# Optimization experiments

Hardware: AMD Instinct MI355X
Metric: run time of the kernel (lower is better)

Reference implementation:

```python
import jax, jax.numpy as jnp
import numpy as np
from jax import lax

NUM_HEADS = 8
EPS = 1e-5  # BatchNorm eps, eval mode with running_mean=0, running_var=1


def _dwconv3x3(x, w):
    # depthwise 3x3, stride 1, pad 1; x: [N,C,H,W], w: [C,1,3,3]
    return lax.conv_general_dilated(x, w, (1, 1), ((1, 1), (1, 1)),
                                    feature_group_count=x.shape[1],
                                    dimension_numbers=('NCHW', 'OIHW', 'NCHW'))


def _bn_eval(x, g, b):
    # eval BN with running stats (0,1): x * g/sqrt(1+eps) + b, channel dim 1
    s = (g * (1.0 / (1.0 + EPS) ** 0.5))
    return x * s[None, :, None, None] + b[None, :, None, None]


def setup_inputs() -> dict:
    key = jax.random.key(0)
    ks = jax.random.split(key, 10)
    B, h, w, C = 2, 16, 16, 128
    T = 1 + h * w
    H = NUM_HEADS
    inp = {
        'x': jax.random.normal(ks[0], (B, T, C), dtype=jnp.float32),
        'attn_score_grad': jax.random.normal(ks[1], (B, H, T, T), dtype=jnp.float32),
        # depthwise conv weights for q/k/v projections
        'dwq_w': jax.random.normal(ks[2], (C, 1, 3, 3), dtype=jnp.float32) * 0.1,
        'dwk_w': jax.random.normal(ks[3], (C, 1, 3, 3), dtype=jnp.float32) * 0.1,
        'dwv_w': jax.random.normal(ks[4], (C, 1, 3, 3), dtype=jnp.float32) * 0.1,
        'bnq_g': jnp.ones((C,), jnp.float32), 'bnq_b': jnp.zeros((C,), jnp.float32),
        'bnk_g': jnp.ones((C,), jnp.float32), 'bnk_b': jnp.zeros((C,), jnp.float32),
        'bnv_g': jnp.ones((C,), jnp.float32), 'bnv_b': jnp.zeros((C,), jnp.float32),
        # linear projections (qkv_bias=False)
        'Wq': jax.random.normal(ks[5], (C, C), dtype=jnp.float32) * (C ** -0.5),
        'Wk': jax.random.normal(ks[6], (C, C), dtype=jnp.float32) * (C ** -0.5),
        'Wv': jax.random.normal(ks[7], (C, C), dtype=jnp.float32) * (C ** -0.5),
        # conv_layer: Conv2d(2C->2C, k3, s2, p1) + BN
        'conv_w': jax.random.normal(ks[8], (2 * C, 2 * C, 3, 3), dtype=jnp.float32) * 0.02,
        'conv_b': jax.random.normal(ks[9], (2 * C,), dtype=jnp.float32) * 0.02,
        'bn2_g': jnp.ones((2 * C,), jnp.float32), 'bn2_b': jnp.zeros((2 * C,), jnp.float32),
        'h': 16, 'w': 16,
    }
    return inp


def reference(x, attn_score_grad, dwq_w, dwk_w, dwv_w, bnq_g, bnq_b, bnk_g, bnk_b,
              bnv_g, bnv_b, Wq, Wk, Wv, conv_w, conv_b, bn2_g, bn2_b, h, w):
    B, T, C = x.shape
    H = NUM_HEADS
    d = C // H
    scale = C ** -0.5  # note: full dim, as in the original

    # forward_conv: split cls token, depthwise conv + BN per q/k/v
    cls = x[:, :1]                                          # [B,1,C]
    xs = x[:, 1:].reshape(B, h, w, C).transpose(0, 3, 1, 2)  # [B,C,h,w]

    def conv_proj(dw, g, b):
        t = _bn_eval(_dwconv3x3(xs, dw), g, b)              # [B,C,h,w]
        return t.transpose(0, 2, 3, 1).reshape(B, h * w, C)

    q = jnp.concatenate([cls, conv_proj(dwq_w, bnq_g, bnq_b)], axis=1)
    k = jnp.concatenate([cls, conv_proj(dwk_w, bnk_g, bnk_b)], axis=1)
    v = jnp.concatenate([cls, conv_proj(dwv_w, bnv_g, bnv_b)], axis=1)

    # linear projections then split heads: b t (h d) -> b h t d
    q = (q @ Wq.T).reshape(B, T, H, d).transpose(0, 2, 1, 3)
    k = (k @ Wk.T).reshape(B, T, H, d).transpose(0, 2, 1, 3)
    v = (v @ Wv.T).reshape(B, T, H, d).transpose(0, 2, 1, 3)

    kv = jnp.concatenate([k, v], axis=-1)                   # [B,H,T,2d]

    # normalize attn_score_grad (temperature-softmax mixture on non-cls part)
    first = attn_score_grad[..., 0:1]
    rem = attn_score_grad[..., 1:]
    pos = jax.nn.softmax(rem / 0.5, axis=-1)
    neg = jax.nn.softmax(-rem / 0.5, axis=-1)
    score = jnp.concatenate([first, 0.7 * pos + 0.3 * (1.0 - neg)], axis=-1)  # [B,H,T,T]

    # weighted_kv[b,h,t1,t2,:] = score[b,h,t1,t2] * kv[b,h,t1,:]
    weighted = score[..., None] * kv[:, :, :, None, :]      # [B,H,T,T,2d]

    cls_tok = weighted[..., :1, :]                          # [B,H,T,1,2d]
    # raw row-major reshape (mixes head into channels), faithful to torch .reshape
    feat = weighted[..., 1:, :].reshape(B, T, h, w, 2 * C)  # [B,T,h,w,2C]
    ci = feat.transpose(0, 1, 4, 2, 3).reshape(B * T, 2 * C, h, w)

    co = lax.conv_general_dilated(ci, conv_w, (2, 2), ((1, 1), (1, 1)),
                                  dimension_numbers=('NCHW', 'OIHW', 'NCHW'))
    co = co + conv_b[None, :, None, None]
    co = _bn_eval(co, bn2_g, bn2_b)                         # [B*T,2C,h/2,w/2]

    co = co.reshape(B, T, H, 2 * d, h // 2, w // 2).transpose(0, 2, 1, 3, 4, 5)
    cf = co.reshape(B, H, T, (h // 2) * (w // 2), 2 * d)    # raw reshape, faithful

    kvps = jnp.concatenate([cls_tok, cf], axis=-2)          # [B,H,T,K,2d]
    k_ps = kvps[..., :d]                                    # [B,H,T,K,d]
    v_ps = kvps[..., d:]

    attn = jax.nn.softmax(jnp.einsum('bhtd,bhtkd->bhtk', q, k_ps) * scale, axis=-1)
    out = jnp.einsum('bhtk,bhtkd->bhtd', attn, v_ps)        # [B,H,T,d]
    out = out.transpose(0, 2, 1, 3).reshape(B, T, C)        # b h t d -> b t (h d)
    return jax.nn.gelu(out, approximate=False)
```

## Files before the change

### kernel.cpp

```cpp
#include <hip/hip_runtime.h>

#define BB 2
#define TT 257
#define CC 128
#define HH 8
#define DD 16
#define C2O 256
#define NIMG (BB*TT)
#define ROWS (BB*HH*TT)
#define KTOT 2304

static __device__ __forceinline__ float wred_max(float v) {
    #pragma unroll
    for (int off = 32; off; off >>= 1) v = fmaxf(v, __shfl_xor(v, off, 64));
    return v;
}
static __device__ __forceinline__ float wred_sum(float v) {
    #pragma unroll
    for (int off = 32; off; off >>= 1) v += __shfl_xor(v, off, 64);
    return v;
}

#define BN_INV 0.9999950000374997f

__global__ void k_pre(const float* __restrict__ x,
                      const float* __restrict__ dwq, const float* __restrict__ dwk, const float* __restrict__ dwv,
                      const float* __restrict__ gq, const float* __restrict__ bq,
                      const float* __restrict__ gk, const float* __restrict__ bk,
                      const float* __restrict__ gv, const float* __restrict__ bv,
                      float* __restrict__ pre) {
    int blk = blockIdx.x;
    int which = blk / NIMG;
    int it = blk - which * NIMG;
    int b = it / TT, t = it - b * TT;
    int c = threadIdx.x;
    const float* dw = (which == 0) ? dwq : (which == 1) ? dwk : dwv;
    const float* g  = (which == 0) ? gq  : (which == 1) ? gk  : gv;
    const float* bi = (which == 0) ? bq  : (which == 1) ? bk  : bv;
    float val;
    if (t == 0) {
        val = x[(b * TT) * CC + c];
    } else {
        int y = (t - 1) >> 4, xx = (t - 1) & 15;
        float s = 0.f;
        #pragma unroll
        for (int ky = 0; ky < 3; ky++) {
            int yy = y + ky - 1;
            if (yy < 0 || yy > 15) continue;
            #pragma unroll
            for (int kx = 0; kx < 3; kx++) {
                int xb = xx + kx - 1;
                if (xb < 0 || xb > 15) continue;
                s += dw[c * 9 + ky * 3 + kx] * x[(b * TT + 1 + yy * 16 + xb) * CC + c];
            }
        }
        val = s * (g[c] * BN_INV) + bi[c];
    }
    pre[(which * NIMG + it) * CC + c] = val;
}

__global__ void k_proj(const float* __restrict__ pre,
                       const float* __restrict__ Wq, const float* __restrict__ Wk, const float* __restrict__ Wv,
                       float* __restrict__ qh, float* __restrict__ kv) {
    int blk = blockIdx.x;
    int which = blk / NIMG;
    int it = blk - which * NIMG;
    int b = it / TT, t = it - b * TT;
    int o = threadIdx.x;
    __shared__ float row[CC];
    row[o] = pre[(which * NIMG + it) * CC + o];
    __syncthreads();
    const float* W = (which == 0) ? Wq : (which == 1) ? Wk : Wv;
    const float* wr = W + o * CC;
    float acc = 0.f;
    #pragma unroll 8
    for (int c = 0; c < CC; c++) acc += wr[c] * row[c];
    int hh = o >> 4, dd = o & 15;
    long ridx = (long)(b * HH + hh) * TT + t;
    if (which == 0)      qh[ridx * DD + dd] = acc;
    else if (which == 1) kv[ridx * 32 + dd] = acc;
    else                 kv[ridx * 32 + 16 + dd] = acc;
}

__global__ void k_score(const float* __restrict__ asg, float* __restrict__ score) {
    int wid = threadIdx.x >> 6;
    int lane = threadIdx.x & 63;
    int r = blockIdx.x * 4 + wid;
    if (r >= ROWS) return;
    const float* src = asg + (long)r * TT;
    float* dst = score + (long)r * TT;
    float e[4];
    #pragma unroll
    for (int i = 0; i < 4; i++) e[i] = src[1 + lane + 64 * i] * 2.0f;
    float mx = fmaxf(fmaxf(e[0], e[1]), fmaxf(e[2], e[3]));
    mx = wred_max(mx);
    float mn = fminf(fminf(e[0], e[1]), fminf(e[2], e[3]));
    mn = -wred_max(-mn);
    float pe[4], ne[4], ps = 0.f, ns = 0.f;
    #pragma unroll
    for (int i = 0; i < 4; i++) {
        pe[i] = expf(e[i] - mx); ps += pe[i];
        ne[i] = expf(mn - e[i]); ns += ne[i];
    }
    ps = wred_sum(ps); ns = wred_sum(ns);
    float rp = 1.f / ps, rn = 1.f / ns;
    #pragma unroll
    for (int i = 0; i < 4; i++)
        dst[1 + lane + 64 * i] = 0.7f * pe[i] * rp + 0.3f * (1.f - ne[i] * rn);
    if (lane == 0) dst[0] = src[0];
}

__global__ void k_w2(const float* __restrict__ cw, float* __restrict__ wt2) {
    int o = blockIdx.x;
    int t = threadIdx.x;
    for (int i = t; i < KTOT; i += 256) {
        int jp = i / 288;
        int r = i - jp * 288;
        int d = r >> 5, v = r & 31;
        wt2[o * KTOT + i] = cw[o * KTOT + (jp * 32 + v) * 9 + d];
    }
}

__launch_bounds__(256, 2)
__global__ void k_fconv(const float* __restrict__ wt2, const float* __restrict__ score,
                        const float* __restrict__ kv, const float* __restrict__ cb,
                        const float* __restrict__ g2, const float* __restrict__ b2,
                        float* __restrict__ cf) {
    __shared__ float s_S[8][256];
    __shared__ float s_kv[8][32];
    __shared__ float s_P[9][8][16][8];
    int bid = blockIdx.x;
    int oc  = bid / NIMG;
    int img = bid - oc * NIMG;
    int b = img / TT, tp = img - b * TT;
    int tid = threadIdx.x;

    {
        int j = tid >> 5, c = tid & 31;
        int m = tp * 8 + j;
        int hh = m / TT, t = m - hh * TT;
        long row = (long)(b * HH + hh) * TT + t;
        s_kv[j][c] = kv[row * 32 + c];
    }
    #pragma unroll
    for (int it = 0; it < 8; it++) {
        int i = tid + 256 * it;
        int j = i >> 8, s = i & 255;
        int m = tp * 8 + j;
        int hh = m / TT, t = m - hh * TT;
        long row = (long)(b * HH + hh) * TT + t;
        s_S[j][s] = score[row * TT + 1 + s];
    }
    __syncthreads();

    {
        int o_l = tid >> 4;
        int jp  = tid & 7;
        int jh  = (tid >> 3) & 1;
        float4 kvr[4][8];
        #pragma unroll
        for (int jj = 0; jj < 4; jj++) {
            const float4* kv4 = (const float4*)(&s_kv[(jh << 2) + jj][0]);
            #pragma unroll
            for (int u = 0; u < 8; u++) kvr[jj][u] = kv4[u];
        }
        const float* gw = wt2 + (((oc << 4) + o_l) * KTOT + jp * 288);
        for (int d = 0; d < 9; d++) {
            const float4* w4 = (const float4*)(gw + (d << 5));
            float4 wv[8];
            #pragma unroll
            for (int u = 0; u < 8; u++) wv[u] = w4[u];
            #pragma unroll
            for (int jj = 0; jj < 4; jj++) {
                float a = 0.f;
                #pragma unroll
                for (int u = 0; u < 8; u++) {
                    a += wv[u].x * kvr[jj][u].x + wv[u].y * kvr[jj][u].y
                       + wv[u].z * kvr[jj][u].z + wv[u].w * kvr[jj][u].w;
                }
                s_P[d][(jh << 2) + jj][o_l][jp] = a;
            }
        }
    }
    __syncthreads();

    int p  = tid >> 2;
    int og = tid & 3;
    int yo = p >> 3, xo = p & 7;
    float acc[4] = {0.f, 0.f, 0.f, 0.f};
    for (int dy = 0; dy < 3; dy++) {
        int y = 2 * yo - 1 + dy;
        if (y < 0) continue;
        int j = y >> 1, ypar = y & 1;
        #pragma unroll
        for (int dx = 0; dx < 3; dx++) {
            int x = 2 * xo - 1 + dx;
            if (x < 0) continue;
            int d = dy * 3 + dx;
            const float4* sp4 = (const float4*)(&s_S[j][(ypar * 16 + x) << 3]);
            float4 s0 = sp4[0], s1 = sp4[1];
            #pragma unroll
            for (int io = 0; io < 4; io++) {
                const float4* pp = (const float4*)(&s_P[d][j][og + (io << 2)][0]);
                float4 p0 = pp[0], p1 = pp[1];
                acc[io] += s0.x * p0.x + s0.y * p0.y + s0.z * p0.z + s0.w * p0.w
                         + s1.x * p1.x + s1.y * p1.y + s1.z * p1.z + s1.w * p1.w;
            }
        }
    }

    int pcf_hi = p >> 5, cp = p & 31;
    #pragma unroll
    for (int io = 0; io < 4; io++) {
        int o = (oc << 4) + og + (io << 2);
        int hh_o = o >> 5, c = o & 31;
        long rowcf = (long)(b * HH + hh_o) * TT + tp;
        int pcf = 2 * c + pcf_hi;
        cf[(rowcf * 64 + pcf) * 32 + cp] = (acc[io] + cb[o]) * (g2[o] * BN_INV) + b2[o];
    }
}

__global__ void k_attn(const float* __restrict__ qh, const float* __restrict__ kv,
                       const float* __restrict__ score, const float* __restrict__ cf,
                       float* __restrict__ out) {
    int row = blockIdx.x;
    int lane = threadIdx.x;
    int b = row / (HH * TT);
    int rem = row - b * (HH * TT);
    int hh = rem / TT, t = rem - hh * TT;
    __shared__ float q[16];
    __shared__ float pv[66];
    __shared__ float vv[65][16];
    if (lane < 16) q[lane] = qh[(long)row * DD + lane];
    __syncthreads();
    const float SCALE = 0.08838834764831845f;
    float d, d2 = -INFINITY;
    if (lane == 0) {
        float s0 = score[(long)row * TT];
        float a = 0.f;
        #pragma unroll
        for (int i = 0; i < 16; i++) {
            float kk = s0 * kv[(long)row * 32 + i];
            a += q[i] * kk;
            vv[0][i] = s0 * kv[(long)row * 32 + 16 + i];
        }
        d = a * SCALE;
        const float* b63 = cf + ((long)row * 64 + 63) * 32;
        a = 0.f;
        #pragma unroll
        for (int i = 0; i < 16; i++) { a += q[i] * b63[i]; vv[64][i] = b63[16 + i]; }
        d2 = a * SCALE;
    } else {
        const float* bp = cf + ((long)row * 64 + (lane - 1)) * 32;
        float a = 0.f;
        #pragma unroll
        for (int i = 0; i < 16; i++) { a += q[i] * bp[i]; vv[lane][i] = bp[16 + i]; }
        d = a * SCALE;
    }
    float mx = wred_max(fmaxf(d, d2));
    float p = expf(d - mx);
    float p2 = (lane == 0) ? expf(d2 - mx) : 0.f;
    float sum = wred_sum(p + p2);
    pv[lane] = p;
    if (lane == 0) pv[64] = p2;
    __syncthreads();
    if (lane < 16) {
        float a = 0.f;
        for (int j = 0; j < 65; j++) a += pv[j] * vv[j][lane];
        float o = a / sum;
        float g = 0.5f * o * (1.f + erff(o * 0.70710678118654752f));
        out[(long)(b * TT + t) * CC + hh * DD + lane] = g;
    }
}

extern "C" void kernel_launch(void* const* d_in, const int* in_sizes, int n_in,
                              void* d_out, int out_size, void* d_ws, size_t ws_size,
                              hipStream_t stream) {
    const float* x   = (const float*)d_in[0];
    const float* asg = (const float*)d_in[1];
    const float* dwq = (const float*)d_in[2];
    const float* dwk = (const float*)d_in[3];
    const float* dwv = (const float*)d_in[4];
    const float* gq  = (const float*)d_in[5];
    const float* bq  = (const float*)d_in[6];
    const float* gk  = (const float*)d_in[7];
    const float* bk  = (const float*)d_in[8];
    const float* gv  = (const float*)d_in[9];
    const float* bv  = (const float*)d_in[10];
    const float* Wq  = (const float*)d_in[11];
    const float* Wk  = (const float*)d_in[12];
    const float* Wv  = (const float*)d_in[13];
    const float* cw  = (const float*)d_in[14];
    const float* cb  = (const float*)d_in[15];
    const float* g2  = (const float*)d_in[16];
    const float* b2  = (const float*)d_in[17];
    float* out = (float*)d_out;

    float* ws = (float*)d_ws;
    float* qh    = ws;
    float* kvv   = qh + 65792;
    float* score = kvv + 131584;
    float* wt2   = score + 1056784;
    float* cf    = wt2 + 589824;
    float* pre   = cf + 8421376;

    k_pre<<<3 * NIMG, CC, 0, stream>>>(x, dwq, dwk, dwv, gq, bq, gk, bk, gv, bv, pre);
    k_proj<<<3 * NIMG, CC, 0, stream>>>(pre, Wq, Wk, Wv, qh, kvv);
    k_score<<<ROWS / 4, 256, 0, stream>>>(asg, score);
    k_w2<<<C2O, 256, 0, stream>>>(cw, wt2);
    k_fconv<<<16 * NIMG, 256, 0, stream>>>(wt2, score, kvv, cb, g2, b2, cf);
    k_attn<<<ROWS, 64, 0, stream>>>(qh, kvv, score, cf, out);
}
```

Before: 411.0 us.

## Interleave weight-projection and conv stages per kernel row to cut shared memory

```diff
diff --git a/kernel.cpp b/kernel.cpp
--- a/kernel.cpp
+++ b/kernel.cpp
@@ -121,14 +121,14 @@
     }
 }
 
-__launch_bounds__(256, 2)
+__launch_bounds__(256, 4)
 __global__ void k_fconv(const float* __restrict__ wt2, const float* __restrict__ score,
                         const float* __restrict__ kv, const float* __restrict__ cb,
                         const float* __restrict__ g2, const float* __restrict__ b2,
                         float* __restrict__ cf) {
-    __shared__ float s_S[8][256];
+    __shared__ float s_S[8][260];
     __shared__ float s_kv[8][32];
-    __shared__ float s_P[9][8][16][8];
+    __shared__ float s_P[3][8][132];
     int bid = blockIdx.x;
     int oc  = bid / NIMG;
     int img = bid - oc * NIMG;
@@ -153,60 +153,72 @@
     }
     __syncthreads();
 
-    {
-        int o_l = tid >> 4;
-        int jp  = tid & 7;
-        int jh  = (tid >> 3) & 1;
-        float4 kvr[4][8];
-        #pragma unroll
-        for (int jj = 0; jj < 4; jj++) {
-            const float4* kv4 = (const float4*)(&s_kv[(jh << 2) + jj][0]);
-            #pragma unroll
-            for (int u = 0; u < 8; u++) kvr[jj][u] = kv4[u];
-        }
-        const float* gw = wt2 + (((oc << 4) + o_l) * KTOT + jp * 288);
-        for (int d = 0; d < 9; d++) {
-            const float4* w4 = (const float4*)(gw + (d << 5));
-            float4 wv[8];
-            #pragma unroll
-            for (int u = 0; u < 8; u++) wv[u] = w4[u];
-            #pragma unroll
-            for (int jj = 0; jj < 4; jj++) {
-                float a = 0.f;
-                #pragma unroll
-                for (int u = 0; u < 8; u++) {
-                    a += wv[u].x * kvr[jj][u].x + wv[u].y * kvr[jj][u].y
-                       + wv[u].z * kvr[jj][u].z + wv[u].w * kvr[jj][u].w;
-                }
-                s_P[d][(jh << 2) + jj][o_l][jp] = a;
-            }
-        }
-    }
-    __syncthreads();
-
+    int o_l = tid >> 4;
+    int jpp = (tid >> 2) & 3;
+    int jq  = tid & 3;
     int p  = tid >> 2;
     int og = tid & 3;
     int yo = p >> 3, xo = p & 7;
+
+    float4 kr[8][2];
+    #pragma unroll
+    for (int j = 0; j < 8; j++) {
+        const float4* p4 = (const float4*)(&s_kv[j][jq << 3]);
+        kr[j][0] = p4[0]; kr[j][1] = p4[1];
+    }
+
+    const float* gw = wt2 + (long)((oc << 4) + o_l) * KTOT + (jpp << 1) * 288 + (jq << 3);
     float acc[4] = {0.f, 0.f, 0.f, 0.f};
+
     for (int dy = 0; dy < 3; dy++) {
-        int y = 2 * yo - 1 + dy;
-        if (y < 0) continue;
-        int j = y >> 1, ypar = y & 1;
         #pragma unroll
         for (int dx = 0; dx < 3; dx++) {
-            int x = 2 * xo - 1 + dx;
-            if (x < 0) continue;
             int d = dy * 3 + dx;
-            const float4* sp4 = (const float4*)(&s_S[j][(ypar * 16 + x) << 3]);
-            float4 s0 = sp4[0], s1 = sp4[1];
             #pragma unroll
-            for (int io = 0; io < 4; io++) {
-                const float4* pp = (const float4*)(&s_P[d][j][og + (io << 2)][0]);
-                float4 p0 = pp[0], p1 = pp[1];
-                acc[io] += s0.x * p0.x + s0.y * p0.y + s0.z * p0.z + s0.w * p0.w
-                         + s1.x * p1.x + s1.y * p1.y + s1.z * p1.z + s1.w * p1.w;
+            for (int jpl = 0; jpl < 2; jpl++) {
+                const float4* w4 = (const float4*)(gw + jpl * 288 + (d << 5));
+                float4 wa = w4[0], wb = w4[1];
+                float part[8];
+                #pragma unroll
+                for (int j = 0; j < 8; j++) {
+                    float4 k0 = kr[j][0], k1 = kr[j][1];
+                    part[j] = wa.x*k0.x + wa.y*k0.y + wa.z*k0.z + wa.w*k0.w
+                            + wb.x*k1.x + wb.y*k1.y + wb.z*k1.z + wb.w*k1.w;
+                }
+                #pragma unroll
+                for (int j = 0; j < 8; j++) {
+                    part[j] += __shfl_xor(part[j], 1, 64);
+                    part[j] += __shfl_xor(part[j], 2, 64);
+                }
+                #pragma unroll
+                for (int i = 0; i < 2; i++) {
+                    float v = (jq == 0) ? part[i] : (jq == 1) ? part[2 + i]
+                            : (jq == 2) ? part[4 + i] : part[6 + i];
+                    int j = (jq << 1) + i;
+                    s_P[dx][j][(o_l << 3) + (jpp << 1) + jpl] = v;
+                }
             }
         }
+        __syncthreads();
+        int y = 2 * yo - 1 + dy;
+        if (y >= 0) {
+            int j = y >> 1, ypar = y & 1;
+            #pragma unroll
+            for (int dx = 0; dx < 3; dx++) {
+                int x = 2 * xo - 1 + dx;
+                if (x < 0) continue;
+                const float4* sp4 = (const float4*)(&s_S[j][((ypar << 4) + x) << 3]);
+                float4 s0 = sp4[0], s1 = sp4[1];
+                #pragma unroll
+                for (int io = 0; io < 4; io++) {
+                    const float4* pp = (const float4*)(&s_P[dx][j][(og + (io << 2)) << 3]);
+                    float4 p0 = pp[0], p1 = pp[1];
+                    acc[io] += s0.x * p0.x + s0.y * p0.y + s0.z * p0.z + s0.w * p0.w
+                             + s1.x * p1.x + s1.y * p1.y + s1.z * p1.z + s1.w * p1.w;
+                }
+            }
+        }
+        __syncthreads();
     }
 
     int pcf_hi = p >> 5, cp = p & 31;
```

Result: faster. 342.4 us (-16.7%).

## Restructure fused conv kernel to stage per-row partials and raise occupancy

Applied to the files above, without the earlier changes.

```diff
diff --git a/kernel.cpp b/kernel.cpp
--- a/kernel.cpp
+++ b/kernel.cpp
@@ -121,92 +121,86 @@
     }
 }
 
-__launch_bounds__(256, 2)
+__launch_bounds__(256, 4)
 __global__ void k_fconv(const float* __restrict__ wt2, const float* __restrict__ score,
                         const float* __restrict__ kv, const float* __restrict__ cb,
                         const float* __restrict__ g2, const float* __restrict__ b2,
                         float* __restrict__ cf) {
-    __shared__ float s_S[8][256];
-    __shared__ float s_kv[8][32];
-    __shared__ float s_P[9][8][16][8];
+    __shared__ float s_S[8][260];
+    __shared__ float s_P[3][8][132];
     int bid = blockIdx.x;
     int oc  = bid / NIMG;
     int img = bid - oc * NIMG;
     int b = img / TT, tp = img - b * TT;
     int tid = threadIdx.x;
 
+    #pragma unroll
+    for (int it = 0; it < 8; it++) {
+        int i = tid + 256 * it;
+        int jj = i >> 8, s = i & 255;
+        int m = tp * 8 + jj;
+        int hh = m / TT, t = m - hh * TT;
+        long row = (long)(b * HH + hh) * TT + t;
+        s_S[jj][s] = score[row * TT + 1 + s];
+    }
+
+    int o_l = tid >> 4;
+    int j   = (tid >> 1) & 7;
+    int rep = tid & 1;
+
+    float4 kr[8];
     {
-        int j = tid >> 5, c = tid & 31;
         int m = tp * 8 + j;
         int hh = m / TT, t = m - hh * TT;
-        long row = (long)(b * HH + hh) * TT + t;
-        s_kv[j][c] = kv[row * 32 + c];
-    }
-    #pragma unroll
-    for (int it = 0; it < 8; it++) {
-        int i = tid + 256 * it;
-        int j = i >> 8, s = i & 255;
-        int m = tp * 8 + j;
-        int hh = m / TT, t = m - hh * TT;
-        long row = (long)(b * HH + hh) * TT + t;
-        s_S[j][s] = score[row * TT + 1 + s];
-    }
-    __syncthreads();
-
-    {
-        int o_l = tid >> 4;
-        int jp  = tid & 7;
-        int jh  = (tid >> 3) & 1;
-        float4 kvr[4][8];
-        #pragma unroll
-        for (int jj = 0; jj < 4; jj++) {
-            const float4* kv4 = (const float4*)(&s_kv[(jh << 2) + jj][0]);
-            #pragma unroll
-            for (int u = 0; u < 8; u++) kvr[jj][u] = kv4[u];
-        }
-        const float* gw = wt2 + (((oc << 4) + o_l) * KTOT + jp * 288);
-        for (int d = 0; d < 9; d++) {
-            const float4* w4 = (const float4*)(gw + (d << 5));
-            float4 wv[8];
-            #pragma unroll
-            for (int u = 0; u < 8; u++) wv[u] = w4[u];
-            #pragma unroll
-            for (int jj = 0; jj < 4; jj++) {
-                float a = 0.f;
-                #pragma unroll
-                for (int u = 0; u < 8; u++) {
-                    a += wv[u].x * kvr[jj][u].x + wv[u].y * kvr[jj][u].y
-                       + wv[u].z * kvr[jj][u].z + wv[u].w * kvr[jj][u].w;
-                }
-                s_P[d][(jh << 2) + jj][o_l][jp] = a;
-            }
-        }
-    }
-    __syncthreads();
+        long krow = (long)(b * HH + hh) * TT + t;
+        const float4* kvg = (const float4*)(kv + krow * 32);
+        #pragma unroll
+        for (int u = 0; u < 8; u++) kr[u] = kvg[u];
+    }
+
+    const float* gw = wt2 + (long)((oc << 4) + o_l) * KTOT + (rep << 2) * 288;
 
     int p  = tid >> 2;
     int og = tid & 3;
     int yo = p >> 3, xo = p & 7;
     float acc[4] = {0.f, 0.f, 0.f, 0.f};
+
+    __syncthreads();
+
     for (int dy = 0; dy < 3; dy++) {
-        int y = 2 * yo - 1 + dy;
-        if (y < 0) continue;
-        int j = y >> 1, ypar = y & 1;
-        #pragma unroll
-        for (int dx = 0; dx < 3; dx++) {
-            int x = 2 * xo - 1 + dx;
-            if (x < 0) continue;
-            int d = dy * 3 + dx;
-            const float4* sp4 = (const float4*)(&s_S[j][(ypar * 16 + x) << 3]);
-            float4 s0 = sp4[0], s1 = sp4[1];
+        for (int jpl = 0; jpl < 4; jpl++) {
             #pragma unroll
-            for (int io = 0; io < 4; io++) {
-                const float4* pp = (const float4*)(&s_P[d][j][og + (io << 2)][0]);
-                float4 p0 = pp[0], p1 = pp[1];
-                acc[io] += s0.x * p0.x + s0.y * p0.y + s0.z * p0.z + s0.w * p0.w
-                         + s1.x * p1.x + s1.y * p1.y + s1.z * p1.z + s1.w * p1.w;
+            for (int dx = 0; dx < 3; dx++) {
+                const float4* w4 = (const float4*)(gw + jpl * 288 + (dy * 3 + dx) * 32);
+                float a = 0.f;
+                #pragma unroll
+                for (int u = 0; u < 8; u++) {
+                    float4 wv = w4[u];
+                    a += wv.x * kr[u].x + wv.y * kr[u].y + wv.z * kr[u].z + wv.w * kr[u].w;
+                }
+                s_P[dx][j][(o_l << 3) + (rep << 2) + jpl] = a;
             }
         }
+        __syncthreads();
+        int y = 2 * yo - 1 + dy;
+        if (y >= 0) {
+            int jj = y >> 1, ypar = y & 1;
+            #pragma unroll
+            for (int dx = 0; dx < 3; dx++) {
+                int x = 2 * xo - 1 + dx;
+                if (x < 0) continue;
+                const float4* sp4 = (const float4*)(&s_S[jj][((ypar << 4) + x) << 3]);
+                float4 s0 = sp4[0], s1 = sp4[1];
+                #pragma unroll
+                for (int io = 0; io < 4; io++) {
+                    const float4* pp = (const float4*)(&s_P[dx][jj][(og + (io << 2)) << 3]);
+                    float4 p0 = pp[0], p1 = pp[1];
+                    acc[io] += s0.x * p0.x + s0.y * p0.y + s0.z * p0.z + s0.w * p0.w
+                             + s1.x * p1.x + s1.y * p1.y + s1.z * p1.z + s1.w * p1.w;
+                }
+            }
+        }
+        __syncthreads();
     }
 
     int pcf_hi = p >> 5, cp = p & 31;
```

New measurement: 776.8 us. 1.89x slower.
